# Performance work log

Measured on AMD Instinct MI355X. Metric: run time of the kernel, lower is better.

## Reference

```python
import jax, jax.numpy as jnp
import numpy as np

B, D, L = 4, 256, 4096

def setup_inputs() -> dict:
    key = jax.random.key(0)
    k1, k2, k3 = jax.random.split(key, 3)
    query = jax.random.normal(k1, (B, D, L), dtype=jnp.float32)
    context = jax.random.normal(k2, (B, D, L), dtype=jnp.float32)
    W_in = jax.random.normal(k3, (D, D), dtype=jnp.float32) * 0.02
    b_in = jnp.zeros((D,), dtype=jnp.float32)
    return {"query": query, "context": context, "W_in": W_in, "b_in": b_in}

def reference(query, context, W_in, b_in):
    # inputs are [B, D, L]; module transposes to [B, L, D]
    q = jnp.transpose(query, (0, 2, 1))    # [B, O, D]
    c = jnp.transpose(context, (0, 2, 1))  # [B, Q, D]
    # 'general': linear_in applied to query only (torch Linear: x @ W^T + b)
    q = q @ W_in.T + b_in
    # unscaled Luong attention: QK^T -> softmax -> A V
    scores = jnp.einsum('bod,bqd->boq', q, c)          # [B, O, Q]
    weights = jax.nn.softmax(scores, axis=-1)          # [B, O, Q]
    out = jnp.einsum('boq,bqd->bod', weights, c)       # [B, O, D]
    return (out, weights)
```

## Files before the change

kernel.cpp:

```cpp
#include <hip/hip_runtime.h>


#define BATCH 4
#define DDIM  256
#define LSEQ  4096
#define TQ    64

typedef float    f32x4 __attribute__((ext_vector_type(4)));
typedef _Float16 f16x8 __attribute__((ext_vector_type(8)));
typedef _Float16 f16x4 __attribute__((ext_vector_type(4)));

__device__ __forceinline__ void gld16(const void* g, void* l) {
  __builtin_amdgcn_global_load_lds((const __attribute__((address_space(1))) void*)g,
                                   (__attribute__((address_space(3))) void*)l, 16, 0, 0);
}

__global__ __launch_bounds__(256) void transpose_cast(
    const float* __restrict__ q_in, const float* __restrict__ c_in,
    _Float16* __restrict__ q_out, _Float16* __restrict__ c_out)
{
  __shared__ float tile[64][68];
  const int which = blockIdx.z >> 2;
  const int b     = blockIdx.z & 3;
  const float* __restrict__ src = which ? c_in : q_in;
  _Float16* __restrict__ dst    = which ? c_out : q_out;
  const int l0 = blockIdx.x * 64, d0 = blockIdx.y * 64;
  const int tid = threadIdx.x;
  const int tr = tid >> 4, tc = (tid & 15) << 2;
#pragma unroll
  for (int i = 0; i < 4; ++i) {
    int d = tr + i * 16;
    f32x4 v = *(const f32x4*)(src + ((size_t)b * DDIM + d0 + d) * LSEQ + l0 + tc);
    *(f32x4*)&tile[d][tc] = v;
  }
  __syncthreads();
#pragma unroll
  for (int i = 0; i < 4; ++i) {
    int l = tr + i * 16;
    f16x4 h;
    h[0] = (_Float16)tile[tc + 0][l];
    h[1] = (_Float16)tile[tc + 1][l];
    h[2] = (_Float16)tile[tc + 2][l];
    h[3] = (_Float16)tile[tc + 3][l];
    *(f16x4*)(dst + ((size_t)b * LSEQ + l0 + l) * DDIM + d0 + tc) = h;
  }
}

__global__ __launch_bounds__(256) void wconv(const float* __restrict__ w,
                                             _Float16* __restrict__ w16) {
  int i = (blockIdx.x * 256 + threadIdx.x) * 4;
  f32x4 v = *(const f32x4*)(w + i);
  f16x4 h;
  h[0] = (_Float16)v[0]; h[1] = (_Float16)v[1];
  h[2] = (_Float16)v[2]; h[3] = (_Float16)v[3];
  *(f16x4*)(w16 + i) = h;
}

__global__ __launch_bounds__(256) void castD(const float* __restrict__ c_in,
                                             _Float16* __restrict__ cD16) {
  size_t i = ((size_t)blockIdx.x * 256 + threadIdx.x) * 8;
  f32x4 a = *(const f32x4*)(c_in + i);
  f32x4 b = *(const f32x4*)(c_in + i + 4);
  f16x8 h;
  h[0] = (_Float16)a[0]; h[1] = (_Float16)a[1];
  h[2] = (_Float16)a[2]; h[3] = (_Float16)a[3];
  h[4] = (_Float16)b[0]; h[5] = (_Float16)b[1];
  h[6] = (_Float16)b[2]; h[7] = (_Float16)b[3];
  *(f16x8*)(cD16 + i) = h;
}

__global__ __launch_bounds__(256) void linear_q(
    const _Float16* __restrict__ qT16, const _Float16* __restrict__ W16,
    const float* __restrict__ bias, _Float16* __restrict__ qw16)
{
  const int tid = threadIdx.x;
  const int wv = tid >> 6, ln = tid & 63, g = ln >> 4, c16 = ln & 15;
  const size_t r0 = (size_t)blockIdx.x * 64 + wv * 16;

  f16x8 qa[8];
  const _Float16* qrow = qT16 + (r0 + c16) * DDIM + g * 8;
#pragma unroll
  for (int kk = 0; kk < 8; ++kk) qa[kk] = *(const f16x8*)(qrow + kk * 32);

  f32x4 acc[16];
#pragma unroll
  for (int n = 0; n < 16; ++n) acc[n] = f32x4{0.f, 0.f, 0.f, 0.f};

#pragma unroll 2
  for (int kk = 0; kk < 8; ++kk) {
#pragma unroll
    for (int n = 0; n < 16; ++n) {
      f16x8 bf = *(const f16x8*)(W16 + (n * 16 + c16) * DDIM + kk * 32 + g * 8);
      acc[n] = __builtin_amdgcn_mfma_f32_16x16x32_f16(qa[kk], bf, acc[n], 0, 0, 0);
    }
  }
#pragma unroll
  for (int n = 0; n < 16; ++n) {
    float bb = bias[n * 16 + c16];
#pragma unroll
    for (int r = 0; r < 4; ++r)
      qw16[(r0 + 4 * g + r) * DDIM + n * 16 + c16] = (_Float16)(acc[n][r] + bb);
  }
}

__global__ __launch_bounds__(512) void attn_main(
    const _Float16* __restrict__ qw16,
    const _Float16* __restrict__ cT16,
    const _Float16* __restrict__ cD16,
    float* __restrict__ outp,
    float* __restrict__ wgt)
{
  __shared__ __align__(16) char smem[2][32768];
  __shared__ __align__(16) char wbuf[8192];
  __shared__ float redbuf[4][64];
  char* obuf = &smem[0][0];

  const int tid = threadIdx.x;
  const int wv  = tid >> 6;
  const int qw  = wv & 3;
  const int oh  = wv >> 2;
  const int ln  = tid & 63;
  const int g   = ln >> 4;
  const int c16 = ln & 15;

  const int lin   = blockIdx.y * 64 + blockIdx.x;
  const int b     = (lin & 7) >> 1;
  const int otile = ((lin >> 3) << 1) | (lin & 1);
  const int o0    = otile * 64;
  const int bo    = b * LSEQ + o0;

  const _Float16* __restrict__ cbase = cT16 + (size_t)b * LSEQ * DDIM;
  const _Float16* __restrict__ cDb   = cD16 + (size_t)b * DDIM * LSEQ;

  f16x8 qb[2][8];
#pragma unroll
  for (int of = 0; of < 2; ++of)
#pragma unroll
    for (int kk = 0; kk < 8; ++kk)
      qb[of][kk] = *(const f16x8*)(qw16 +
          ((size_t)(bo + oh * 32 + of * 16 + c16) << 8) + kk * 32 + g * 8);

  auto issue_dma = [&](int t, int pp) {
#pragma unroll
    for (int i = 0; i < 4; ++i) {
      unsigned x  = (unsigned)tid * 16 + i * 8192;
      unsigned q  = x >> 9;
      unsigned db = (x & 511u) ^ ((q & 7u) << 4);
      gld16(cbase + ((size_t)(t * TQ + q) << 8) + (db >> 1), &smem[pp][x]);
    }
  };

  float lsum0 = 0.f, lsum1 = 0.f;
  int p = 0;
  issue_dma(0, 0);
  for (int t = 0; t < LSEQ / TQ; ++t) {
    asm volatile("s_waitcnt vmcnt(0)" ::: "memory");
    __builtin_amdgcn_s_barrier();
    issue_dma(t < LSEQ / TQ - 1 ? t + 1 : 0, p ^ 1);
    __builtin_amdgcn_sched_barrier(0);

    const char* cl = smem[p];
    f32x4 sa0{0.f, 0.f, 0.f, 0.f}, sa1{0.f, 0.f, 0.f, 0.f};
#pragma unroll
    for (int kk = 0; kk < 8; ++kk) {
      unsigned off = (unsigned)((qw * 16 + c16) * 512 + kk * 64 + g * 16) ^
                     ((unsigned)(c16 & 7) << 4);
      f16x8 af = *(const f16x8*)(cl + off);
      sa0 = __builtin_amdgcn_mfma_f32_16x16x32_f16(af, qb[0][kk], sa0, 0, 0, 0);
      sa1 = __builtin_amdgcn_mfma_f32_16x16x32_f16(af, qb[1][kk], sa1, 0, 0, 0);
    }
#pragma unroll
    for (int r = 0; r < 4; ++r) {
      lsum0 += __expf(sa0[r]);
      lsum1 += __expf(sa1[r]);
    }
    p ^= 1;
  }

  lsum0 += __shfl_xor(lsum0, 16); lsum0 += __shfl_xor(lsum0, 32);
  lsum1 += __shfl_xor(lsum1, 16); lsum1 += __shfl_xor(lsum1, 32);
  if (ln < 16) {
    redbuf[qw][oh * 32 + ln]      = lsum0;
    redbuf[qw][oh * 32 + 16 + ln] = lsum1;
  }
  __syncthreads();
  float invl[2];
#pragma unroll
  for (int of = 0; of < 2; ++of) {
    int o = oh * 32 + of * 16 + c16;
    invl[of] = 1.0f / (redbuf[0][o] + redbuf[1][o] + redbuf[2][o] + redbuf[3][o]);
  }

  f32x4 oacc[4][4];
#pragma unroll
  for (int m = 0; m < 4; ++m)
#pragma unroll
    for (int nf = 0; nf < 4; ++nf) oacc[m][nf] = f32x4{0.f, 0.f, 0.f, 0.f};

  for (int t = 0; t < LSEQ / TQ; ++t) {
    const int q0 = t * TQ;
    if (t == 0) asm volatile("s_waitcnt vmcnt(0)" ::: "memory");
    else        asm volatile("s_waitcnt vmcnt(2)" ::: "memory");
    __builtin_amdgcn_s_barrier();
    __builtin_amdgcn_sched_barrier(0);

    f16x8 bv[4];
#pragma unroll
    for (int nf = 0; nf < 4; ++nf)
      bv[nf] = *(const f16x8*)(cDb +
          ((size_t)(qw * 64 + nf * 16 + c16) << 12) + q0 + oh * 32 + g * 8);

    if (t < LSEQ / TQ - 1) issue_dma(t + 1, p ^ 1);

    const char* cl = smem[p];
    f32x4 sa0{0.f, 0.f, 0.f, 0.f}, sa1{0.f, 0.f, 0.f, 0.f};
#pragma unroll
    for (int kk = 0; kk < 8; ++kk) {
      unsigned off = (unsigned)((qw * 16 + c16) * 512 + kk * 64 + g * 16) ^
                     ((unsigned)(c16 & 7) << 4);
      f16x8 af = *(const f16x8*)(cl + off);
      sa0 = __builtin_amdgcn_mfma_f32_16x16x32_f16(af, qb[0][kk], sa0, 0, 0, 0);
      sa1 = __builtin_amdgcn_mfma_f32_16x16x32_f16(af, qb[1][kk], sa1, 0, 0, 0);
    }

#pragma unroll
    for (int of = 0; of < 2; ++of) {
      f32x4 sv = of ? sa1 : sa0;
      f32x4 wv4;
      f16x4 wh;
#pragma unroll
      for (int r = 0; r < 4; ++r) {
        float w = __expf(sv[r]) * invl[of];
        wv4[r] = w;
        wh[r]  = (_Float16)w;
      }
      int o = oh * 32 + of * 16 + c16;
      *(f32x4*)(wgt + ((size_t)(bo + o) << 12) + q0 + qw * 16 + 4 * g) = wv4;
      unsigned wb = (unsigned)(o * 128 + qw * 32 + g * 8) ^ ((unsigned)(o & 7) << 4);
      *(f16x4*)(wbuf + wb) = wh;
    }
    asm volatile("s_waitcnt lgkmcnt(0)" ::: "memory");
    __builtin_amdgcn_s_barrier();
    __builtin_amdgcn_sched_barrier(0);

#pragma unroll
    for (int m = 0; m < 4; ++m) {
      unsigned off = (unsigned)((m * 16 + c16) * 128 + oh * 64 + g * 16) ^
                     ((unsigned)(c16 & 7) << 4);
      f16x8 wa = *(const f16x8*)(wbuf + off);
#pragma unroll
      for (int nf = 0; nf < 4; ++nf)
        oacc[m][nf] =
            __builtin_amdgcn_mfma_f32_16x16x32_f16(wa, bv[nf], oacc[m][nf], 0, 0, 0);
    }
    p ^= 1;
  }

  __syncthreads();
  if (oh == 1) {
#pragma unroll
    for (int m = 0; m < 4; ++m)
#pragma unroll
      for (int nf = 0; nf < 4; ++nf)
        *(f32x4*)(obuf + qw * 16384 + (m * 4 + nf) * 1024 + ln * 16) = oacc[m][nf];
  }
  __syncthreads();
  if (oh == 0) {
#pragma unroll
    for (int m = 0; m < 4; ++m)
#pragma unroll
      for (int nf = 0; nf < 4; ++nf) {
        f32x4 o2 = *(const f32x4*)(obuf + qw * 16384 + (m * 4 + nf) * 1024 + ln * 16);
        f32x4 o  = oacc[m][nf] + o2;
#pragma unroll
        for (int r = 0; r < 4; ++r)
          outp[((size_t)(bo + m * 16 + 4 * g + r) << 8) + qw * 64 + nf * 16 + c16] = o[r];
      }
  }
}

extern "C" void kernel_launch(void* const* d_in, const int* in_sizes, int n_in,
                              void* d_out, int out_size, void* d_ws, size_t ws_size,
                              hipStream_t stream) {
  const float* query   = (const float*)d_in[0];
  const float* context = (const float*)d_in[1];
  const float* W_in    = (const float*)d_in[2];
  const float* b_in    = (const float*)d_in[3];

  float* outp = (float*)d_out;
  float* wgt  = outp + (size_t)BATCH * LSEQ * DDIM;

  const size_t NELEM = (size_t)BATCH * LSEQ * DDIM;
  _Float16* qT16 = (_Float16*)d_ws;
  _Float16* cT16 = qT16 + NELEM;
  _Float16* qw16 = cT16 + NELEM;
  _Float16* W16  = qw16 + NELEM;
  _Float16* cD16 = qT16;

  transpose_cast<<<dim3(LSEQ / 64, DDIM / 64, 2 * BATCH), 256, 0, stream>>>(
      query, context, qT16, cT16);
  wconv<<<(DDIM * DDIM) / 1024, 256, 0, stream>>>(W_in, W16);
  linear_q<<<(BATCH * LSEQ) / 64, 256, 0, stream>>>(qT16, W16, b_in, qw16);
  castD<<<(int)(NELEM / 2048), 256, 0, stream>>>(context, cD16);
  attn_main<<<dim3(64, BATCH), 512, 0, stream>>>(qw16, cT16, cD16, outp, wgt);
}
```

Before: 271.2 us.

## Fuse context fp16 cast into transpose and double attention waves per block

The separate castD kernel is removed, and transpose_cast now also writes the non-transposed fp16 copy of context while it already holds the data in registers. This saves one full read of context and one kernel launch. attn_main goes from 8 to 16 waves per block: each wave now owns 16 query rows instead of 32 for scores, and a 32-wide D slice for the output GEMM. This gives more latency hiding but duplicates the LDS reads of context tiles across twice as many waves and raises register pressure with launch_bounds(1024). The cD16 buffer moves to its own workspace region because qT16 is still needed when the cast now happens earlier.

```diff
diff --git a/kernel.cpp b/kernel.cpp
--- a/kernel.cpp
+++ b/kernel.cpp
@@ -17,7 +17,8 @@
 
 __global__ __launch_bounds__(256) void transpose_cast(
     const float* __restrict__ q_in, const float* __restrict__ c_in,
-    _Float16* __restrict__ q_out, _Float16* __restrict__ c_out)
+    _Float16* __restrict__ q_out, _Float16* __restrict__ c_out,
+    _Float16* __restrict__ cD16)
 {
   __shared__ float tile[64][68];
   const int which = blockIdx.z >> 2;
@@ -32,6 +33,12 @@
     int d = tr + i * 16;
     f32x4 v = *(const f32x4*)(src + ((size_t)b * DDIM + d0 + d) * LSEQ + l0 + tc);
     *(f32x4*)&tile[d][tc] = v;
+    if (which) {
+      f16x4 h;
+      h[0] = (_Float16)v[0]; h[1] = (_Float16)v[1];
+      h[2] = (_Float16)v[2]; h[3] = (_Float16)v[3];
+      *(f16x4*)(cD16 + ((size_t)b * DDIM + d0 + d) * LSEQ + l0 + tc) = h;
+    }
   }
   __syncthreads();
 #pragma unroll
@@ -56,19 +63,6 @@
   *(f16x4*)(w16 + i) = h;
 }
 
-__global__ __launch_bounds__(256) void castD(const float* __restrict__ c_in,
-                                             _Float16* __restrict__ cD16) {
-  size_t i = ((size_t)blockIdx.x * 256 + threadIdx.x) * 8;
-  f32x4 a = *(const f32x4*)(c_in + i);
-  f32x4 b = *(const f32x4*)(c_in + i + 4);
-  f16x8 h;
-  h[0] = (_Float16)a[0]; h[1] = (_Float16)a[1];
-  h[2] = (_Float16)a[2]; h[3] = (_Float16)a[3];
-  h[4] = (_Float16)b[0]; h[5] = (_Float16)b[1];
-  h[6] = (_Float16)b[2]; h[7] = (_Float16)b[3];
-  *(f16x8*)(cD16 + i) = h;
-}
-
 __global__ __launch_bounds__(256) void linear_q(
     const _Float16* __restrict__ qT16, const _Float16* __restrict__ W16,
     const float* __restrict__ bias, _Float16* __restrict__ qw16)
@@ -103,7 +97,7 @@
   }
 }
 
-__global__ __launch_bounds__(512) void attn_main(
+__global__ __launch_bounds__(1024, 4) void attn_main(
     const _Float16* __restrict__ qw16,
     const _Float16* __restrict__ cT16,
     const _Float16* __restrict__ cD16,
@@ -118,7 +112,9 @@
   const int tid = threadIdx.x;
   const int wv  = tid >> 6;
   const int qw  = wv & 3;
-  const int oh  = wv >> 2;
+  const int ow  = wv >> 2;
+  const int kh  = wv & 1;
+  const int dw  = wv >> 1;
   const int ln  = tid & 63;
   const int g   = ln >> 4;
   const int c16 = ln & 15;
@@ -132,25 +128,23 @@
   const _Float16* __restrict__ cbase = cT16 + (size_t)b * LSEQ * DDIM;
   const _Float16* __restrict__ cDb   = cD16 + (size_t)b * DDIM * LSEQ;
 
-  f16x8 qb[2][8];
-#pragma unroll
-  for (int of = 0; of < 2; ++of)
-#pragma unroll
-    for (int kk = 0; kk < 8; ++kk)
-      qb[of][kk] = *(const f16x8*)(qw16 +
-          ((size_t)(bo + oh * 32 + of * 16 + c16) << 8) + kk * 32 + g * 8);
+  f16x8 qb[8];
+#pragma unroll
+  for (int kk = 0; kk < 8; ++kk)
+    qb[kk] = *(const f16x8*)(qw16 +
+        ((size_t)(bo + ow * 16 + c16) << 8) + kk * 32 + g * 8);
 
   auto issue_dma = [&](int t, int pp) {
 #pragma unroll
-    for (int i = 0; i < 4; ++i) {
-      unsigned x  = (unsigned)tid * 16 + i * 8192;
+    for (int i = 0; i < 2; ++i) {
+      unsigned x  = (unsigned)tid * 16 + i * 16384;
       unsigned q  = x >> 9;
       unsigned db = (x & 511u) ^ ((q & 7u) << 4);
       gld16(cbase + ((size_t)(t * TQ + q) << 8) + (db >> 1), &smem[pp][x]);
     }
   };
 
-  float lsum0 = 0.f, lsum1 = 0.f;
+  float lsum = 0.f;
   int p = 0;
   issue_dma(0, 0);
   for (int t = 0; t < LSEQ / TQ; ++t) {
@@ -160,83 +154,70 @@
     __builtin_amdgcn_sched_barrier(0);
 
     const char* cl = smem[p];
-    f32x4 sa0{0.f, 0.f, 0.f, 0.f}, sa1{0.f, 0.f, 0.f, 0.f};
+    f32x4 sa{0.f, 0.f, 0.f, 0.f};
 #pragma unroll
     for (int kk = 0; kk < 8; ++kk) {
       unsigned off = (unsigned)((qw * 16 + c16) * 512 + kk * 64 + g * 16) ^
                      ((unsigned)(c16 & 7) << 4);
       f16x8 af = *(const f16x8*)(cl + off);
-      sa0 = __builtin_amdgcn_mfma_f32_16x16x32_f16(af, qb[0][kk], sa0, 0, 0, 0);
-      sa1 = __builtin_amdgcn_mfma_f32_16x16x32_f16(af, qb[1][kk], sa1, 0, 0, 0);
-    }
-#pragma unroll
-    for (int r = 0; r < 4; ++r) {
-      lsum0 += __expf(sa0[r]);
-      lsum1 += __expf(sa1[r]);
-    }
+      sa = __builtin_amdgcn_mfma_f32_16x16x32_f16(af, qb[kk], sa, 0, 0, 0);
+    }
+#pragma unroll
+    for (int r = 0; r < 4; ++r) lsum += __expf(sa[r]);
     p ^= 1;
   }
 
-  lsum0 += __shfl_xor(lsum0, 16); lsum0 += __shfl_xor(lsum0, 32);
-  lsum1 += __shfl_xor(lsum1, 16); lsum1 += __shfl_xor(lsum1, 32);
-  if (ln < 16) {
-    redbuf[qw][oh * 32 + ln]      = lsum0;
-    redbuf[qw][oh * 32 + 16 + ln] = lsum1;
-  }
-  __syncthreads();
-  float invl[2];
-#pragma unroll
-  for (int of = 0; of < 2; ++of) {
-    int o = oh * 32 + of * 16 + c16;
-    invl[of] = 1.0f / (redbuf[0][o] + redbuf[1][o] + redbuf[2][o] + redbuf[3][o]);
-  }
-
-  f32x4 oacc[4][4];
+  lsum += __shfl_xor(lsum, 16);
+  lsum += __shfl_xor(lsum, 32);
+  if (ln < 16) redbuf[qw][ow * 16 + ln] = lsum;
+  __syncthreads();
+  const int o_mine = ow * 16 + c16;
+  const float invl = 1.0f / (redbuf[0][o_mine] + redbuf[1][o_mine] +
+                             redbuf[2][o_mine] + redbuf[3][o_mine]);
+
+  f32x4 oacc[4][2];
 #pragma unroll
   for (int m = 0; m < 4; ++m)
 #pragma unroll
-    for (int nf = 0; nf < 4; ++nf) oacc[m][nf] = f32x4{0.f, 0.f, 0.f, 0.f};
+    for (int nf = 0; nf < 2; ++nf) oacc[m][nf] = f32x4{0.f, 0.f, 0.f, 0.f};
 
   for (int t = 0; t < LSEQ / TQ; ++t) {
     const int q0 = t * TQ;
     if (t == 0) asm volatile("s_waitcnt vmcnt(0)" ::: "memory");
-    else        asm volatile("s_waitcnt vmcnt(2)" ::: "memory");
+    else        asm volatile("s_waitcnt vmcnt(1)" ::: "memory");
     __builtin_amdgcn_s_barrier();
     __builtin_amdgcn_sched_barrier(0);
 
-    f16x8 bv[4];
-#pragma unroll
-    for (int nf = 0; nf < 4; ++nf)
+    f16x8 bv[2];
+#pragma unroll
+    for (int nf = 0; nf < 2; ++nf)
       bv[nf] = *(const f16x8*)(cDb +
-          ((size_t)(qw * 64 + nf * 16 + c16) << 12) + q0 + oh * 32 + g * 8);
+          ((size_t)(dw * 32 + nf * 16 + c16) << 12) + q0 + kh * 32 + g * 8);
 
     if (t < LSEQ / TQ - 1) issue_dma(t + 1, p ^ 1);
 
     const char* cl = smem[p];
-    f32x4 sa0{0.f, 0.f, 0.f, 0.f}, sa1{0.f, 0.f, 0.f, 0.f};
+    f32x4 sa{0.f, 0.f, 0.f, 0.f};
 #pragma unroll
     for (int kk = 0; kk < 8; ++kk) {
       unsigned off = (unsigned)((qw * 16 + c16) * 512 + kk * 64 + g * 16) ^
                      ((unsigned)(c16 & 7) << 4);
       f16x8 af = *(const f16x8*)(cl + off);
-      sa0 = __builtin_amdgcn_mfma_f32_16x16x32_f16(af, qb[0][kk], sa0, 0, 0, 0);
-      sa1 = __builtin_amdgcn_mfma_f32_16x16x32_f16(af, qb[1][kk], sa1, 0, 0, 0);
-    }
-
-#pragma unroll
-    for (int of = 0; of < 2; ++of) {
-      f32x4 sv = of ? sa1 : sa0;
+      sa = __builtin_amdgcn_mfma_f32_16x16x32_f16(af, qb[kk], sa, 0, 0, 0);
+    }
+
+    {
       f32x4 wv4;
       f16x4 wh;
 #pragma unroll
       for (int r = 0; r < 4; ++r) {
-        float w = __expf(sv[r]) * invl[of];
+        float w = __expf(sa[r]) * invl;
         wv4[r] = w;
         wh[r]  = (_Float16)w;
       }
-      int o = oh * 32 + of * 16 + c16;
-      *(f32x4*)(wgt + ((size_t)(bo + o) << 12) + q0 + qw * 16 + 4 * g) = wv4;
-      unsigned wb = (unsigned)(o * 128 + qw * 32 + g * 8) ^ ((unsigned)(o & 7) << 4);
+      *(f32x4*)(wgt + ((size_t)(bo + o_mine) << 12) + q0 + qw * 16 + 4 * g) = wv4;
+      unsigned wb = (unsigned)(o_mine * 128 + (qw * 16 + 4 * g) * 2) ^
+                    ((unsigned)(o_mine & 7) << 4);
       *(f16x4*)(wbuf + wb) = wh;
     }
     asm volatile("s_waitcnt lgkmcnt(0)" ::: "memory");
@@ -245,11 +226,11 @@
 
 #pragma unroll
     for (int m = 0; m < 4; ++m) {
-      unsigned off = (unsigned)((m * 16 + c16) * 128 + oh * 64 + g * 16) ^
+      unsigned off = (unsigned)((m * 16 + c16) * 128 + kh * 64 + g * 16) ^
                      ((unsigned)(c16 & 7) << 4);
       f16x8 wa = *(const f16x8*)(wbuf + off);
 #pragma unroll
-      for (int nf = 0; nf < 4; ++nf)
+      for (int nf = 0; nf < 2; ++nf)
         oacc[m][nf] =
             __builtin_amdgcn_mfma_f32_16x16x32_f16(wa, bv[nf], oacc[m][nf], 0, 0, 0);
     }
@@ -257,24 +238,24 @@
   }
 
   __syncthreads();
-  if (oh == 1) {
+  if (kh == 1) {
 #pragma unroll
     for (int m = 0; m < 4; ++m)
 #pragma unroll
-      for (int nf = 0; nf < 4; ++nf)
-        *(f32x4*)(obuf + qw * 16384 + (m * 4 + nf) * 1024 + ln * 16) = oacc[m][nf];
-  }
-  __syncthreads();
-  if (oh == 0) {
+      for (int nf = 0; nf < 2; ++nf)
+        *(f32x4*)(obuf + dw * 8192 + (m * 2 + nf) * 1024 + ln * 16) = oacc[m][nf];
+  }
+  __syncthreads();
+  if (kh == 0) {
 #pragma unroll
     for (int m = 0; m < 4; ++m)
 #pragma unroll
-      for (int nf = 0; nf < 4; ++nf) {
-        f32x4 o2 = *(const f32x4*)(obuf + qw * 16384 + (m * 4 + nf) * 1024 + ln * 16);
+      for (int nf = 0; nf < 2; ++nf) {
+        f32x4 o2 = *(const f32x4*)(obuf + dw * 8192 + (m * 2 + nf) * 1024 + ln * 16);
         f32x4 o  = oacc[m][nf] + o2;
 #pragma unroll
         for (int r = 0; r < 4; ++r)
-          outp[((size_t)(bo + m * 16 + 4 * g + r) << 8) + qw * 64 + nf * 16 + c16] = o[r];
+          outp[((size_t)(bo + m * 16 + 4 * g + r) << 8) + dw * 32 + nf * 16 + c16] = o[r];
       }
   }
 }
@@ -295,12 +276,11 @@
   _Float16* cT16 = qT16 + NELEM;
   _Float16* qw16 = cT16 + NELEM;
   _Float16* W16  = qw16 + NELEM;
-  _Float16* cD16 = qT16;
+  _Float16* cD16 = W16 + 65536;
 
   transpose_cast<<<dim3(LSEQ / 64, DDIM / 64, 2 * BATCH), 256, 0, stream>>>(
-      query, context, qT16, cT16);
+      query, context, qT16, cT16, cD16);
   wconv<<<(DDIM * DDIM) / 1024, 256, 0, stream>>>(W_in, W16);
   linear_q<<<(BATCH * LSEQ) / 64, 256, 0, stream>>>(qT16, W16, b_in, qw16);
-  castD<<<(int)(NELEM / 2048), 256, 0, stream>>>(context, cD16);
-  attn_main<<<dim3(64, BATCH), 512, 0, stream>>>(qw16, cT16, cD16, outp, wgt);
-}
+  attn_main<<<dim3(64, BATCH), 1024, 0, stream>>>(qw16, cT16, cD16, outp, wgt);
+}
```

Result: no change. 266.7 us (-1.7%).
